# Optimization experiments

Measured on AMD Instinct MI355X. Metric: run time of the kernel, lower is better.

## Reference

```python
import jax, jax.numpy as jnp
import numpy as np

N_HEAD = 16

def setup_inputs() -> dict:
    key = jax.random.key(0)
    k1, k2, k3 = jax.random.split(key, 3)
    B, T, C = 2, 2048, 1024
    x_norm_for_qk = jax.random.normal(k1, (B, T, C), dtype=jnp.float32)
    xt_current_for_v = jax.random.normal(k2, (B, T, C), dtype=jnp.float32)
    W_attn = jax.random.normal(k3, (C, 2 * C), dtype=jnp.float32) * (1.0 / np.sqrt(C))
    b_attn = jnp.zeros((2 * C,), dtype=jnp.float32)
    return {"x_norm_for_qk": x_norm_for_qk, "xt_current_for_v": xt_current_for_v,
            "W_attn": W_attn, "b_attn": b_attn}

def reference(x_norm_for_qk, xt_current_for_v, W_attn, b_attn):
    B, T, C = x_norm_for_qk.shape
    H = N_HEAD
    D = C // H  # head dim
    qk = x_norm_for_qk @ W_attn + b_attn          # [B,T,2C]
    q, k = qk[..., :C], qk[..., C:]
    q = q.reshape(B, T, H, D).transpose(0, 2, 1, 3)   # [B,H,T,D]
    k = k.reshape(B, T, H, D).transpose(0, 2, 1, 3)
    v = xt_current_for_v.reshape(B, T, H, D).transpose(0, 2, 1, 3)
    scale = 1.0 / np.sqrt(D).astype(np.float32)
    scores = jnp.einsum('bhqd,bhkd->bhqk', q, k) * scale  # [B,H,T,T]
    causal = jnp.tril(jnp.ones((T, T), dtype=bool))
    scores = jnp.where(causal[None, None], scores, jnp.float32(-jnp.inf))
    weights = jax.nn.softmax(scores, axis=-1)  # dropout p=0.0 -> identity
    y = jnp.einsum('bhqk,bhkd->bhqd', weights, v)
    return y.transpose(0, 2, 1, 3).reshape(B, T, C)
```

## Files before the change

kernel.cpp:

```cpp
#include <hip/hip_runtime.h>
#include <hip/hip_bf16.h>
#include <math.h>

typedef __attribute__((ext_vector_type(8))) short s8v;
typedef __attribute__((ext_vector_type(4))) float f4v;
typedef __attribute__((ext_vector_type(16))) float f16v;
typedef __attribute__((ext_vector_type(2))) unsigned int u32x2;
typedef unsigned short ush;
typedef unsigned int u32;

#define QSCALE 0.180336880f
#define FIXED_M 10.0f

static __device__ __forceinline__ ush f2bf(float f) {
    u32 x = __builtin_bit_cast(u32, f);
    return (ush)((x + 0x7fffu + ((x >> 16) & 1u)) >> 16);
}
static __device__ __forceinline__ u32 bfpack(float lo, float hi) {
    u32 a = __builtin_bit_cast(u32, lo) + 0x8000u;
    u32 b = __builtin_bit_cast(u32, hi) + 0x8000u;
    return __builtin_amdgcn_perm(b, a, 0x07060302);
}
static __device__ __forceinline__ void gl_lds16(const void* g, void* l) {
    __builtin_amdgcn_global_load_lds(
        (const __attribute__((address_space(1))) u32*)g,
        (__attribute__((address_space(3))) u32*)l, 16, 0, 0);
}
#if __has_builtin(__builtin_amdgcn_exp2f)
#define EXP2F(x) __builtin_amdgcn_exp2f(x)
#else
#define EXP2F(x) exp2f(x)
#endif

static __device__ __forceinline__ void pl32swap(u32& a, u32& b) {
#if __has_builtin(__builtin_amdgcn_permlane32_swap)
    u32x2 r = __builtin_amdgcn_permlane32_swap(a, b, false, false);
    a = r[0]; b = r[1];
#else
    asm volatile("v_permlane32_swap_b32 %0, %1" : "+v"(a), "+v"(b));
#endif
}
static __device__ __forceinline__ s8v mkfrag(u32 a, u32 b, u32 c, u32 d) {
    union { u32 w[4]; s8v v; } u;
    u.w[0] = a; u.w[1] = b; u.w[2] = c; u.w[3] = d;
    return u.v;
}

static __device__ __forceinline__ void softpack(
    const f16v& s0, const f16v& s1, bool needmask, int kbase, int qg,
    float& lr, s8v& pf0, s8v& pf1, s8v& pf2, s8v& pf3)
{
    float ps = 0.f;
    u32 w0[4], w1[4], x0[4], x1[4];
    if (needmask) {
        #pragma unroll
        for (int g4 = 0; g4 < 4; ++g4) {
            const int kb0 = kbase + 8 * g4;
            float e0a = (kb0 + 0 > qg) ? 0.f : EXP2F(s0[g4 * 4 + 0] - FIXED_M);
            float e0b = (kb0 + 1 > qg) ? 0.f : EXP2F(s0[g4 * 4 + 1] - FIXED_M);
            float e0c = (kb0 + 2 > qg) ? 0.f : EXP2F(s0[g4 * 4 + 2] - FIXED_M);
            float e0d = (kb0 + 3 > qg) ? 0.f : EXP2F(s0[g4 * 4 + 3] - FIXED_M);
            float e1a = (kb0 + 32 > qg) ? 0.f : EXP2F(s1[g4 * 4 + 0] - FIXED_M);
            float e1b = (kb0 + 33 > qg) ? 0.f : EXP2F(s1[g4 * 4 + 1] - FIXED_M);
            float e1c = (kb0 + 34 > qg) ? 0.f : EXP2F(s1[g4 * 4 + 2] - FIXED_M);
            float e1d = (kb0 + 35 > qg) ? 0.f : EXP2F(s1[g4 * 4 + 3] - FIXED_M);
            ps += (e0a + e0b) + (e0c + e0d) + (e1a + e1b) + (e1c + e1d);
            w0[g4] = bfpack(e0a, e0b); w1[g4] = bfpack(e0c, e0d);
            x0[g4] = bfpack(e1a, e1b); x1[g4] = bfpack(e1c, e1d);
        }
    } else {
        #pragma unroll
        for (int g4 = 0; g4 < 4; ++g4) {
            float e0a = EXP2F(s0[g4 * 4 + 0] - FIXED_M);
            float e0b = EXP2F(s0[g4 * 4 + 1] - FIXED_M);
            float e0c = EXP2F(s0[g4 * 4 + 2] - FIXED_M);
            float e0d = EXP2F(s0[g4 * 4 + 3] - FIXED_M);
            float e1a = EXP2F(s1[g4 * 4 + 0] - FIXED_M);
            float e1b = EXP2F(s1[g4 * 4 + 1] - FIXED_M);
            float e1c = EXP2F(s1[g4 * 4 + 2] - FIXED_M);
            float e1d = EXP2F(s1[g4 * 4 + 3] - FIXED_M);
            ps += (e0a + e0b) + (e0c + e0d) + (e1a + e1b) + (e1c + e1d);
            w0[g4] = bfpack(e0a, e0b); w1[g4] = bfpack(e0c, e0d);
            x0[g4] = bfpack(e1a, e1b); x1[g4] = bfpack(e1c, e1d);
        }
    }
    ps += __shfl_xor(ps, 32);
    lr += ps;
    pl32swap(w0[0], w0[1]); pl32swap(w1[0], w1[1]);
    pl32swap(w0[2], w0[3]); pl32swap(w1[2], w1[3]);
    pl32swap(x0[0], x0[1]); pl32swap(x1[0], x1[1]);
    pl32swap(x0[2], x0[3]); pl32swap(x1[2], x1[3]);
    pf0 = mkfrag(w0[0], w1[0], w0[1], w1[1]);
    pf1 = mkfrag(w0[2], w1[2], w0[3], w1[3]);
    pf2 = mkfrag(x0[0], x1[0], x0[1], x1[1]);
    pf3 = mkfrag(x0[2], x1[2], x0[3], x1[3]);
}

__global__ __launch_bounds__(256) void prep_kernel(
    const float* __restrict__ X, const float* __restrict__ W,
    const float* __restrict__ XV,
    ush* __restrict__ Xb, ush* __restrict__ Wt, ush* __restrict__ Vtb)
{
    __shared__ float Ts[64][68];
    const int tid = threadIdx.x;
    const int bid = blockIdx.x;
    if (bid < 2048) {
        const size_t i = ((size_t)bid * 256 + tid) * 8;
        float4 v0 = *(const float4*)(X + i);
        float4 v1 = *(const float4*)(X + i + 4);
        uint4 o;
        o.x = bfpack(v0.x, v0.y); o.y = bfpack(v0.z, v0.w);
        o.z = bfpack(v1.x, v1.y); o.w = bfpack(v1.z, v1.w);
        *(uint4*)(Xb + i) = o;
    } else if (bid < 2560) {
        const int id = bid - 2048;
        const int n0 = (id & 31) * 64, k0 = (id >> 5) * 64;
        #pragma unroll
        for (int p = 0; p < 4; ++p) {
            const int idx = p * 256 + tid;
            const int kr = idx >> 4, nc4 = idx & 15;
            float4 v = *(const float4*)(W + (size_t)(k0 + kr) * 2048 + n0 + nc4 * 4);
            Ts[kr][nc4 * 4 + 0] = v.x; Ts[kr][nc4 * 4 + 1] = v.y;
            Ts[kr][nc4 * 4 + 2] = v.z; Ts[kr][nc4 * 4 + 3] = v.w;
        }
        __syncthreads();
        const int n = tid >> 2, kb = (tid & 3) * 16;
        #pragma unroll
        for (int p = 0; p < 4; ++p) {
            const int k = kb + p * 4;
            ushort4 o;
            o.x = f2bf(Ts[k + 0][n]); o.y = f2bf(Ts[k + 1][n]);
            o.z = f2bf(Ts[k + 2][n]); o.w = f2bf(Ts[k + 3][n]);
            *(ushort4*)(Wt + (size_t)(n0 + n) * 1024 + k0 + k) = o;
        }
    } else {
        const int id = bid - 2560;
        const int t0 = (id & 31) * 64;
        const int bh = id >> 5;
        const int b = bh >> 4, h = bh & 15;
        #pragma unroll
        for (int p = 0; p < 4; ++p) {
            const int idx = p * 256 + tid;
            const int tr = idx >> 4, dc4 = idx & 15;
            float4 v = *(const float4*)(XV + (size_t)(b * 2048 + t0 + tr) * 1024
                                        + h * 64 + dc4 * 4);
            Ts[tr][dc4 * 4 + 0] = v.x; Ts[tr][dc4 * 4 + 1] = v.y;
            Ts[tr][dc4 * 4 + 2] = v.z; Ts[tr][dc4 * 4 + 3] = v.w;
        }
        __syncthreads();
        const int d = tid >> 2, tb = (tid & 3) * 16;
        #pragma unroll
        for (int p = 0; p < 4; ++p) {
            const int tq = tb + p * 4;
            ushort4 o;
            o.x = f2bf(Ts[tq + 0][d]); o.y = f2bf(Ts[tq + 1][d]);
            o.z = f2bf(Ts[tq + 2][d]); o.w = f2bf(Ts[tq + 3][d]);
            *(ushort4*)(Vtb + (size_t)((b * 16 + h) * 64 + d) * 2048 + t0 + tq) = o;
        }
    }
}

__global__ __launch_bounds__(256) void gemm_kernel(
    const ush* __restrict__ Xb, const ush* __restrict__ Wt,
    const float* __restrict__ bias,
    ush* __restrict__ Qb, ush* __restrict__ Kb)
{
    __shared__ ush As[128 * 32];
    __shared__ ush Bs[128 * 32];

    const int tid = threadIdx.x;
    const int wid = tid >> 6, lane = tid & 63;
    const int quad = lane >> 4, l15 = lane & 15;
    const int wm = wid >> 1, wn = wid & 1;
    const int m0 = blockIdx.y * 128, n0 = blockIdx.x * 128;

    const int lrow = lane >> 2;
    const int lkk = (lane & 3) * 8;
    const size_t arow = (size_t)(m0 + wid * 32 + lrow);
    const size_t brow = (size_t)(n0 + wid * 32 + lrow);
    ush* AsW = &As[wid * 1024];
    ush* BsW = &Bs[wid * 1024];

    f4v acc[4][4];
    #pragma unroll
    for (int i = 0; i < 4; ++i)
        #pragma unroll
        for (int j = 0; j < 4; ++j) acc[i][j] = (f4v){0.f, 0.f, 0.f, 0.f};

    for (int k0 = 0; k0 < 1024; k0 += 32) {
        gl_lds16(Xb + arow * 1024 + k0 + lkk, AsW);
        gl_lds16(Xb + (arow + 16) * 1024 + k0 + lkk, AsW + 512);
        gl_lds16(Wt + brow * 1024 + k0 + lkk, BsW);
        gl_lds16(Wt + (brow + 16) * 1024 + k0 + lkk, BsW + 512);
        __syncthreads();

        s8v a[4], bf[4];
        #pragma unroll
        for (int i = 0; i < 4; ++i)
            a[i] = *(const s8v*)&As[(wm * 64 + i * 16 + l15) * 32 + quad * 8];
        #pragma unroll
        for (int j = 0; j < 4; ++j)
            bf[j] = *(const s8v*)&Bs[(wn * 64 + j * 16 + l15) * 32 + quad * 8];
        #pragma unroll
        for (int i = 0; i < 4; ++i)
            #pragma unroll
            for (int j = 0; j < 4; ++j)
                acc[i][j] = __builtin_amdgcn_mfma_f32_16x16x32_bf16(
                    a[i], bf[j], acc[i][j], 0, 0, 0);
        __syncthreads();
    }

    #pragma unroll
    for (int j = 0; j < 4; ++j) {
        const int n = n0 + wn * 64 + j * 16 + l15;
        const float bv = bias[n];
        const bool is_k = n >= 1024;
        const int nn = n & 1023;
        const int h = nn >> 6, d = nn & 63;
        ush* dst = is_k ? Kb : Qb;
        #pragma unroll
        for (int i = 0; i < 4; ++i) {
            const int mrow = m0 + wm * 64 + i * 16 + quad * 4;
            #pragma unroll
            for (int r = 0; r < 4; ++r) {
                const int m = mrow + r;
                const int b = m >> 11, t = m & 2047;
                float val = acc[i][j][r] + bv;
                if (!is_k) val *= QSCALE;
                dst[(size_t)((b * 16 + h) * 2048 + t) * 64 + d] = f2bf(val);
            }
        }
    }
}

__global__ __launch_bounds__(256, 2) void attn_kernel(
    const ush* __restrict__ Qb, const ush* __restrict__ Kb,
    const ush* __restrict__ Vt, float* __restrict__ Y)
{
    __shared__ ush SMEM[32768];
    ush* Kbuf = SMEM;
    ush* Vbuf = SMEM + 16384;

    const int tid = threadIdx.x;
    const int w = tid >> 6, lane = tid & 63;
    const int l31 = lane & 31, hi = lane >> 5;

    const int idx = blockIdx.x;
    const int half = idx >> 8, pair = idx & 255;
    const int qt = half ? (pair & 15) : 15 - (pair & 15);
    const int bh = (pair >> 4) + half * 16;
    const int b = bh >> 4, h = bh & 15;
    const int q0 = qt * 128;
    const int ktmax = 2 * qt + 1;

    const ush* Qg = Qb + (size_t)bh * 2048 * 64;
    const ush* Kg = Kb + (size_t)bh * 2048 * 64;
    const ush* Vg = Vt + (size_t)bh * 64 * 2048;

    ush* Pw = SMEM + w * 2304;
    {
        const int r8q = lane >> 3, c8 = lane & 7;
        #pragma unroll
        for (int p = 0; p < 4; ++p) {
            const int row = p * 8 + r8q;
            uint4 v = *(const uint4*)(Qg + (size_t)(q0 + w * 32 + row) * 64 + c8 * 8);
            *(uint4*)&Pw[row * 72 + c8 * 8] = v;
        }
    }
    s8v bq[4];
    #pragma unroll
    for (int s = 0; s < 4; ++s)
        bq[s] = *(const s8v*)&Pw[l31 * 72 + s * 16 + hi * 8];
    __syncthreads();

    const int r8 = lane >> 3;
    const int g8 = ((lane & 7) ^ r8) * 8;
    auto stage = [&](int kt) {
        const int buf = kt & 3;
        const int k0e = kt * 64;
        const ush* kg = Kg + (size_t)(k0e + w * 16 + r8) * 64 + g8;
        gl_lds16(kg, &Kbuf[buf * 4096 + (w * 16) * 64]);
        gl_lds16(kg + 8 * 64, &Kbuf[buf * 4096 + (w * 16 + 8) * 64]);
        const ush* vg = Vg + (size_t)(w * 16 + r8) * 2048 + k0e + g8;
        gl_lds16(vg, &Vbuf[buf * 4096 + (w * 16) * 64]);
        gl_lds16(vg + 8 * 2048, &Vbuf[buf * 4096 + (w * 16 + 8) * 64]);
    };

    f16v acco0 = {}, acco1 = {};
    float lr = 0.f;
    const int qg = q0 + w * 32 + l31;
    const int qwmax = q0 + w * 32 + 31;

    stage(0); stage(1);
    asm volatile("s_waitcnt vmcnt(4)" ::: "memory");
    __builtin_amdgcn_s_barrier();
    __builtin_amdgcn_sched_barrier(0);

    for (int kt = 0; kt <= ktmax; ++kt) {
        const int sl = (kt & 3) * 4096;
        const bool active = (kt * 64) <= qwmax;
        const bool pf = (kt + 2 <= ktmax);

        s8v ak0[4], ak1[4], av0[4], av1[4];
        if (active) {
            #pragma unroll
            for (int s = 0; s < 4; ++s) {
                const int ch = (s << 1) + hi;
                const int row0 = l31, row1 = 32 + l31;
                ak0[s] = *(const s8v*)&Kbuf[sl + row0 * 64 + ((ch ^ (row0 & 7)) << 3)];
                ak1[s] = *(const s8v*)&Kbuf[sl + row1 * 64 + ((ch ^ (row1 & 7)) << 3)];
                av0[s] = *(const s8v*)&Vbuf[sl + row0 * 64 + ((ch ^ (row0 & 7)) << 3)];
                av1[s] = *(const s8v*)&Vbuf[sl + row1 * 64 + ((ch ^ (row1 & 7)) << 3)];
            }
        }
        __builtin_amdgcn_sched_barrier(0);

        if (pf) stage(kt + 2);

        if (active) {
            f16v s0 = {}, s1 = {};
            #pragma unroll
            for (int s = 0; s < 4; ++s) {
                s0 = __builtin_amdgcn_mfma_f32_32x32x16_bf16(ak0[s], bq[s], s0, 0, 0, 0);
                s1 = __builtin_amdgcn_mfma_f32_32x32x16_bf16(ak1[s], bq[s], s1, 0, 0, 0);
            }

            s8v pf0, pf1, pf2, pf3;
            softpack(s0, s1, (kt * 64 + 63) > (q0 + w * 32),
                     kt * 64 + 4 * hi, qg, lr, pf0, pf1, pf2, pf3);

            acco0 = __builtin_amdgcn_mfma_f32_32x32x16_bf16(av0[0], pf0, acco0, 0, 0, 0);
            acco1 = __builtin_amdgcn_mfma_f32_32x32x16_bf16(av1[0], pf0, acco1, 0, 0, 0);
            acco0 = __builtin_amdgcn_mfma_f32_32x32x16_bf16(av0[1], pf1, acco0, 0, 0, 0);
            acco1 = __builtin_amdgcn_mfma_f32_32x32x16_bf16(av1[1], pf1, acco1, 0, 0, 0);
            acco0 = __builtin_amdgcn_mfma_f32_32x32x16_bf16(av0[2], pf2, acco0, 0, 0, 0);
            acco1 = __builtin_amdgcn_mfma_f32_32x32x16_bf16(av1[2], pf2, acco1, 0, 0, 0);
            acco0 = __builtin_amdgcn_mfma_f32_32x32x16_bf16(av0[3], pf3, acco0, 0, 0, 0);
            acco1 = __builtin_amdgcn_mfma_f32_32x32x16_bf16(av1[3], pf3, acco1, 0, 0, 0);
        }

        if (pf) asm volatile("s_waitcnt vmcnt(4)" ::: "memory");
        else    asm volatile("s_waitcnt vmcnt(0)" ::: "memory");
        __builtin_amdgcn_s_barrier();
        __builtin_amdgcn_sched_barrier(0);
    }

    float* LTw = (float*)SMEM + w * (32 * 68);
    const float inv = 1.0f / lr;
    #pragma unroll
    for (int r = 0; r < 16; ++r) {
        const int d = (r & 3) + 8 * (r >> 2) + 4 * hi;
        LTw[l31 * 68 + d] = acco0[r] * inv;
        LTw[l31 * 68 + 32 + d] = acco1[r] * inv;
    }
    const int qr4 = lane >> 4, chk = lane & 15;
    #pragma unroll
    for (int p = 0; p < 8; ++p) {
        const int qrow = p * 4 + qr4;
        f4v v = *(const f4v*)&LTw[qrow * 68 + chk * 4];
        *(float4*)(Y + (size_t)(b * 2048 + q0 + w * 32 + qrow) * 1024
                   + h * 64 + chk * 4) = (float4){v[0], v[1], v[2], v[3]};
    }
}

extern "C" void kernel_launch(void* const* d_in, const int* in_sizes, int n_in,
                              void* d_out, int out_size, void* d_ws,
                              size_t ws_size, hipStream_t stream)
{
    const float* x_qk = (const float*)d_in[0];
    const float* x_v  = (const float*)d_in[1];
    const float* W    = (const float*)d_in[2];
    const float* bias = (const float*)d_in[3];
    float* out = (float*)d_out;

    unsigned char* ws = (unsigned char*)d_ws;
    ush* Xb = (ush*)(ws);
    ush* Wt = (ush*)(ws + (8u << 20));
    ush* Qb = (ush*)(ws + (12u << 20));
    ush* Kb = (ush*)(ws + (20u << 20));
    ush* Vt = (ush*)(ws + (28u << 20));

    prep_kernel<<<3584, 256, 0, stream>>>(x_qk, W, x_v, Xb, Wt, Vt);
    gemm_kernel<<<dim3(16, 32), 256, 0, stream>>>(Xb, Wt, bias, Qb, Kb);
    attn_kernel<<<512, 256, 0, stream>>>(Qb, Kb, Vt, out);
}
```

Before: 148.7 us.

## Restructure attention into single-wave blocks loading K/V directly into registers

The attention kernel changes from 256-thread blocks with 128-query tiles and LDS-staged, 4-buffered K/V to 2048 one-wave blocks that each handle 32 queries. K and V fragments are now loaded straight from global memory into registers with a two-deep register double-buffer, which drops the LDS staging and block barriers. A new block-to-tile mapping interleaves long and short causal tiles to balance load. The trade-off is that K/V are no longer shared through LDS across waves, so global/L2 traffic per query rises, and the small blocks may hide latency less well.

```diff
diff --git a/kernel.cpp b/kernel.cpp
--- a/kernel.cpp
+++ b/kernel.cpp
@@ -44,56 +44,6 @@
     union { u32 w[4]; s8v v; } u;
     u.w[0] = a; u.w[1] = b; u.w[2] = c; u.w[3] = d;
     return u.v;
-}
-
-static __device__ __forceinline__ void softpack(
-    const f16v& s0, const f16v& s1, bool needmask, int kbase, int qg,
-    float& lr, s8v& pf0, s8v& pf1, s8v& pf2, s8v& pf3)
-{
-    float ps = 0.f;
-    u32 w0[4], w1[4], x0[4], x1[4];
-    if (needmask) {
-        #pragma unroll
-        for (int g4 = 0; g4 < 4; ++g4) {
-            const int kb0 = kbase + 8 * g4;
-            float e0a = (kb0 + 0 > qg) ? 0.f : EXP2F(s0[g4 * 4 + 0] - FIXED_M);
-            float e0b = (kb0 + 1 > qg) ? 0.f : EXP2F(s0[g4 * 4 + 1] - FIXED_M);
-            float e0c = (kb0 + 2 > qg) ? 0.f : EXP2F(s0[g4 * 4 + 2] - FIXED_M);
-            float e0d = (kb0 + 3 > qg) ? 0.f : EXP2F(s0[g4 * 4 + 3] - FIXED_M);
-            float e1a = (kb0 + 32 > qg) ? 0.f : EXP2F(s1[g4 * 4 + 0] - FIXED_M);
-            float e1b = (kb0 + 33 > qg) ? 0.f : EXP2F(s1[g4 * 4 + 1] - FIXED_M);
-            float e1c = (kb0 + 34 > qg) ? 0.f : EXP2F(s1[g4 * 4 + 2] - FIXED_M);
-            float e1d = (kb0 + 35 > qg) ? 0.f : EXP2F(s1[g4 * 4 + 3] - FIXED_M);
-            ps += (e0a + e0b) + (e0c + e0d) + (e1a + e1b) + (e1c + e1d);
-            w0[g4] = bfpack(e0a, e0b); w1[g4] = bfpack(e0c, e0d);
-            x0[g4] = bfpack(e1a, e1b); x1[g4] = bfpack(e1c, e1d);
-        }
-    } else {
-        #pragma unroll
-        for (int g4 = 0; g4 < 4; ++g4) {
-            float e0a = EXP2F(s0[g4 * 4 + 0] - FIXED_M);
-            float e0b = EXP2F(s0[g4 * 4 + 1] - FIXED_M);
-            float e0c = EXP2F(s0[g4 * 4 + 2] - FIXED_M);
-            float e0d = EXP2F(s0[g4 * 4 + 3] - FIXED_M);
-            float e1a = EXP2F(s1[g4 * 4 + 0] - FIXED_M);
-            float e1b = EXP2F(s1[g4 * 4 + 1] - FIXED_M);
-            float e1c = EXP2F(s1[g4 * 4 + 2] - FIXED_M);
-            float e1d = EXP2F(s1[g4 * 4 + 3] - FIXED_M);
-            ps += (e0a + e0b) + (e0c + e0d) + (e1a + e1b) + (e1c + e1d);
-            w0[g4] = bfpack(e0a, e0b); w1[g4] = bfpack(e0c, e0d);
-            x0[g4] = bfpack(e1a, e1b); x1[g4] = bfpack(e1c, e1d);
-        }
-    }
-    ps += __shfl_xor(ps, 32);
-    lr += ps;
-    pl32swap(w0[0], w0[1]); pl32swap(w1[0], w1[1]);
-    pl32swap(w0[2], w0[3]); pl32swap(w1[2], w1[3]);
-    pl32swap(x0[0], x0[1]); pl32swap(x1[0], x1[1]);
-    pl32swap(x0[2], x0[3]); pl32swap(x1[2], x1[3]);
-    pf0 = mkfrag(w0[0], w1[0], w0[1], w1[1]);
-    pf1 = mkfrag(w0[2], w1[2], w0[3], w1[3]);
-    pf2 = mkfrag(x0[0], x1[0], x0[1], x1[1]);
-    pf3 = mkfrag(x0[2], x1[2], x0[3], x1[3]);
 }
 
 __global__ __launch_bounds__(256) void prep_kernel(
@@ -233,132 +183,126 @@
     }
 }
 
-__global__ __launch_bounds__(256, 2) void attn_kernel(
+__global__ __launch_bounds__(64, 2) void attn_kernel(
     const ush* __restrict__ Qb, const ush* __restrict__ Kb,
     const ush* __restrict__ Vt, float* __restrict__ Y)
 {
-    __shared__ ush SMEM[32768];
-    ush* Kbuf = SMEM;
-    ush* Vbuf = SMEM + 16384;
-
-    const int tid = threadIdx.x;
-    const int w = tid >> 6, lane = tid & 63;
+    __shared__ float LT[32 * 68];
+
+    const int lane = threadIdx.x;
     const int l31 = lane & 31, hi = lane >> 5;
 
     const int idx = blockIdx.x;
-    const int half = idx >> 8, pair = idx & 255;
-    const int qt = half ? (pair & 15) : 15 - (pair & 15);
-    const int bh = (pair >> 4) + half * 16;
+    const int g = idx >> 8, c = idx & 255;
+    const int r = c & 7, bh = c >> 3;
+    const int qt = (g < 4) ? (63 - (4 * r + g)) : (4 * r + (g - 4));
     const int b = bh >> 4, h = bh & 15;
-    const int q0 = qt * 128;
-    const int ktmax = 2 * qt + 1;
+    const int q0 = qt * 32;
+    const int nt = qt + 1;
 
     const ush* Qg = Qb + (size_t)bh * 2048 * 64;
     const ush* Kg = Kb + (size_t)bh * 2048 * 64;
     const ush* Vg = Vt + (size_t)bh * 64 * 2048;
 
-    ush* Pw = SMEM + w * 2304;
+    s8v bq[4];
     {
-        const int r8q = lane >> 3, c8 = lane & 7;
-        #pragma unroll
-        for (int p = 0; p < 4; ++p) {
-            const int row = p * 8 + r8q;
-            uint4 v = *(const uint4*)(Qg + (size_t)(q0 + w * 32 + row) * 64 + c8 * 8);
-            *(uint4*)&Pw[row * 72 + c8 * 8] = v;
-        }
-    }
-    s8v bq[4];
-    #pragma unroll
-    for (int s = 0; s < 4; ++s)
-        bq[s] = *(const s8v*)&Pw[l31 * 72 + s * 16 + hi * 8];
-    __syncthreads();
-
-    const int r8 = lane >> 3;
-    const int g8 = ((lane & 7) ^ r8) * 8;
-    auto stage = [&](int kt) {
-        const int buf = kt & 3;
-        const int k0e = kt * 64;
-        const ush* kg = Kg + (size_t)(k0e + w * 16 + r8) * 64 + g8;
-        gl_lds16(kg, &Kbuf[buf * 4096 + (w * 16) * 64]);
-        gl_lds16(kg + 8 * 64, &Kbuf[buf * 4096 + (w * 16 + 8) * 64]);
-        const ush* vg = Vg + (size_t)(w * 16 + r8) * 2048 + k0e + g8;
-        gl_lds16(vg, &Vbuf[buf * 4096 + (w * 16) * 64]);
-        gl_lds16(vg + 8 * 2048, &Vbuf[buf * 4096 + (w * 16 + 8) * 64]);
+        const ush* qb = Qg + (size_t)(q0 + l31) * 64 + hi * 8;
+        bq[0] = *(const s8v*)(qb);
+        bq[1] = *(const s8v*)(qb + 16);
+        bq[2] = *(const s8v*)(qb + 32);
+        bq[3] = *(const s8v*)(qb + 48);
+    }
+
+    f16v acc0 = {}, acc1 = {};
+    float lr = 0.f;
+    const int qg = q0 + l31;
+
+    auto ldK = [&](int kt, s8v* ak) {
+        const ush* kb = Kg + (size_t)(kt * 32 + l31) * 64 + hi * 8;
+        ak[0] = *(const s8v*)(kb);
+        ak[1] = *(const s8v*)(kb + 16);
+        ak[2] = *(const s8v*)(kb + 32);
+        ak[3] = *(const s8v*)(kb + 48);
     };
-
-    f16v acco0 = {}, acco1 = {};
-    float lr = 0.f;
-    const int qg = q0 + w * 32 + l31;
-    const int qwmax = q0 + w * 32 + 31;
-
-    stage(0); stage(1);
-    asm volatile("s_waitcnt vmcnt(4)" ::: "memory");
-    __builtin_amdgcn_s_barrier();
-    __builtin_amdgcn_sched_barrier(0);
-
-    for (int kt = 0; kt <= ktmax; ++kt) {
-        const int sl = (kt & 3) * 4096;
-        const bool active = (kt * 64) <= qwmax;
-        const bool pf = (kt + 2 <= ktmax);
-
-        s8v ak0[4], ak1[4], av0[4], av1[4];
-        if (active) {
+    auto ldV = [&](int kt, s8v* av) {
+        const ush* vb0 = Vg + (size_t)l31 * 2048 + kt * 32 + hi * 8;
+        const ush* vb1 = vb0 + 32 * 2048;
+        av[0] = *(const s8v*)(vb0);
+        av[1] = *(const s8v*)(vb0 + 16);
+        av[2] = *(const s8v*)(vb1);
+        av[3] = *(const s8v*)(vb1 + 16);
+    };
+
+    auto comp = [&](int kt, const s8v* ak, const s8v* av) {
+        f16v s0 = {};
+        #pragma unroll
+        for (int s = 0; s < 4; ++s)
+            s0 = __builtin_amdgcn_mfma_f32_32x32x16_bf16(ak[s], bq[s], s0, 0, 0, 0);
+
+        float ps = 0.f;
+        u32 w0[4], w1[4];
+        if (kt == qt) {
+            const int kbase = kt * 32 + 4 * hi;
             #pragma unroll
-            for (int s = 0; s < 4; ++s) {
-                const int ch = (s << 1) + hi;
-                const int row0 = l31, row1 = 32 + l31;
-                ak0[s] = *(const s8v*)&Kbuf[sl + row0 * 64 + ((ch ^ (row0 & 7)) << 3)];
-                ak1[s] = *(const s8v*)&Kbuf[sl + row1 * 64 + ((ch ^ (row1 & 7)) << 3)];
-                av0[s] = *(const s8v*)&Vbuf[sl + row0 * 64 + ((ch ^ (row0 & 7)) << 3)];
-                av1[s] = *(const s8v*)&Vbuf[sl + row1 * 64 + ((ch ^ (row1 & 7)) << 3)];
+            for (int g4 = 0; g4 < 4; ++g4) {
+                const int kb0 = kbase + 8 * g4;
+                float e0a = (kb0 + 0 > qg) ? 0.f : EXP2F(s0[g4 * 4 + 0] - FIXED_M);
+                float e0b = (kb0 + 1 > qg) ? 0.f : EXP2F(s0[g4 * 4 + 1] - FIXED_M);
+                float e0c = (kb0 + 2 > qg) ? 0.f : EXP2F(s0[g4 * 4 + 2] - FIXED_M);
+                float e0d = (kb0 + 3 > qg) ? 0.f : EXP2F(s0[g4 * 4 + 3] - FIXED_M);
+                ps += (e0a + e0b) + (e0c + e0d);
+                w0[g4] = bfpack(e0a, e0b); w1[g4] = bfpack(e0c, e0d);
             }
-        }
-        __builtin_amdgcn_sched_barrier(0);
-
-        if (pf) stage(kt + 2);
-
-        if (active) {
-            f16v s0 = {}, s1 = {};
+        } else {
             #pragma unroll
-            for (int s = 0; s < 4; ++s) {
-                s0 = __builtin_amdgcn_mfma_f32_32x32x16_bf16(ak0[s], bq[s], s0, 0, 0, 0);
-                s1 = __builtin_amdgcn_mfma_f32_32x32x16_bf16(ak1[s], bq[s], s1, 0, 0, 0);
+            for (int g4 = 0; g4 < 4; ++g4) {
+                float e0a = EXP2F(s0[g4 * 4 + 0] - FIXED_M);
+                float e0b = EXP2F(s0[g4 * 4 + 1] - FIXED_M);
+                float e0c = EXP2F(s0[g4 * 4 + 2] - FIXED_M);
+                float e0d = EXP2F(s0[g4 * 4 + 3] - FIXED_M);
+                ps += (e0a + e0b) + (e0c + e0d);
+                w0[g4] = bfpack(e0a, e0b); w1[g4] = bfpack(e0c, e0d);
             }
-
-            s8v pf0, pf1, pf2, pf3;
-            softpack(s0, s1, (kt * 64 + 63) > (q0 + w * 32),
-                     kt * 64 + 4 * hi, qg, lr, pf0, pf1, pf2, pf3);
-
-            acco0 = __builtin_amdgcn_mfma_f32_32x32x16_bf16(av0[0], pf0, acco0, 0, 0, 0);
-            acco1 = __builtin_amdgcn_mfma_f32_32x32x16_bf16(av1[0], pf0, acco1, 0, 0, 0);
-            acco0 = __builtin_amdgcn_mfma_f32_32x32x16_bf16(av0[1], pf1, acco0, 0, 0, 0);
-            acco1 = __builtin_amdgcn_mfma_f32_32x32x16_bf16(av1[1], pf1, acco1, 0, 0, 0);
-            acco0 = __builtin_amdgcn_mfma_f32_32x32x16_bf16(av0[2], pf2, acco0, 0, 0, 0);
-            acco1 = __builtin_amdgcn_mfma_f32_32x32x16_bf16(av1[2], pf2, acco1, 0, 0, 0);
-            acco0 = __builtin_amdgcn_mfma_f32_32x32x16_bf16(av0[3], pf3, acco0, 0, 0, 0);
-            acco1 = __builtin_amdgcn_mfma_f32_32x32x16_bf16(av1[3], pf3, acco1, 0, 0, 0);
-        }
-
-        if (pf) asm volatile("s_waitcnt vmcnt(4)" ::: "memory");
-        else    asm volatile("s_waitcnt vmcnt(0)" ::: "memory");
-        __builtin_amdgcn_s_barrier();
-        __builtin_amdgcn_sched_barrier(0);
-    }
-
-    float* LTw = (float*)SMEM + w * (32 * 68);
+        }
+        ps += __shfl_xor(ps, 32);
+        lr += ps;
+
+        pl32swap(w0[0], w0[1]); pl32swap(w1[0], w1[1]);
+        pl32swap(w0[2], w0[3]); pl32swap(w1[2], w1[3]);
+        s8v pf0 = mkfrag(w0[0], w1[0], w0[1], w1[1]);
+        s8v pf1 = mkfrag(w0[2], w1[2], w0[3], w1[3]);
+
+        acc0 = __builtin_amdgcn_mfma_f32_32x32x16_bf16(av[0], pf0, acc0, 0, 0, 0);
+        acc1 = __builtin_amdgcn_mfma_f32_32x32x16_bf16(av[2], pf0, acc1, 0, 0, 0);
+        acc0 = __builtin_amdgcn_mfma_f32_32x32x16_bf16(av[1], pf1, acc0, 0, 0, 0);
+        acc1 = __builtin_amdgcn_mfma_f32_32x32x16_bf16(av[3], pf1, acc1, 0, 0, 0);
+    };
+
+    s8v akA[4], avA[4], akB[4], avB[4];
+    ldK(0, akA); ldV(0, avA);
+    for (int kt = 0; kt < nt; kt += 2) {
+        const bool hasB = (kt + 1 < nt);
+        if (hasB) { ldK(kt + 1, akB); ldV(kt + 1, avB); }
+        comp(kt, akA, avA);
+        if (hasB) {
+            if (kt + 2 < nt) { ldK(kt + 2, akA); ldV(kt + 2, avA); }
+            comp(kt + 1, akB, avB);
+        }
+    }
+
     const float inv = 1.0f / lr;
     #pragma unroll
-    for (int r = 0; r < 16; ++r) {
-        const int d = (r & 3) + 8 * (r >> 2) + 4 * hi;
-        LTw[l31 * 68 + d] = acco0[r] * inv;
-        LTw[l31 * 68 + 32 + d] = acco1[r] * inv;
+    for (int r2 = 0; r2 < 16; ++r2) {
+        const int d = (r2 & 3) + 8 * (r2 >> 2) + 4 * hi;
+        LT[l31 * 68 + d] = acc0[r2] * inv;
+        LT[l31 * 68 + 32 + d] = acc1[r2] * inv;
     }
     const int qr4 = lane >> 4, chk = lane & 15;
     #pragma unroll
     for (int p = 0; p < 8; ++p) {
         const int qrow = p * 4 + qr4;
-        f4v v = *(const f4v*)&LTw[qrow * 68 + chk * 4];
-        *(float4*)(Y + (size_t)(b * 2048 + q0 + w * 32 + qrow) * 1024
+        f4v v = *(const f4v*)&LT[qrow * 68 + chk * 4];
+        *(float4*)(Y + (size_t)(b * 2048 + q0 + qrow) * 1024
                    + h * 64 + chk * 4) = (float4){v[0], v[1], v[2], v[3]};
     }
 }
@@ -382,5 +326,5 @@
 
     prep_kernel<<<3584, 256, 0, stream>>>(x_qk, W, x_v, Xb, Wt, Vt);
     gemm_kernel<<<dim3(16, 32), 256, 0, stream>>>(Xb, Wt, bias, Qb, Kb);
-    attn_kernel<<<512, 256, 0, stream>>>(Qb, Kb, Vt, out);
-}
+    attn_kernel<<<2048, 64, 0, stream>>>(Qb, Kb, Vt, out);
+}
```

Measured after the change: 180.9 us. 21.7% more time.

## Multi-buffer GEMM LDS tiles and prefetch two k-steps ahead

Applied to the files above, without the earlier changes.

Replaces the single-buffered load/sync/compute loop of the QK projection GEMM with a 4-slot LDS ring that issues global-to-LDS loads two iterations ahead and waits with explicit vmcnt counters and one barrier per step. The goal is to overlap global memory latency with MFMA work. It raises LDS use to 64KB per block and adds launch bounds of 2 blocks per CU, which may limit occupancy or register allocation. Correctness depends on the hand-tuned waitcnt values matching the number of outstanding loads.

```diff
diff --git a/kernel.cpp b/kernel.cpp
--- a/kernel.cpp
+++ b/kernel.cpp
@@ -160,13 +160,13 @@
     }
 }
 
-__global__ __launch_bounds__(256) void gemm_kernel(
+__global__ __launch_bounds__(256, 2) void gemm_kernel(
     const ush* __restrict__ Xb, const ush* __restrict__ Wt,
     const float* __restrict__ bias,
     ush* __restrict__ Qb, ush* __restrict__ Kb)
 {
-    __shared__ ush As[128 * 32];
-    __shared__ ush Bs[128 * 32];
+    __shared__ ush As[4][128 * 32];
+    __shared__ ush Bs[4][128 * 32];
 
     const int tid = threadIdx.x;
     const int wid = tid >> 6, lane = tid & 63;
@@ -178,8 +178,14 @@
     const int lkk = (lane & 3) * 8;
     const size_t arow = (size_t)(m0 + wid * 32 + lrow);
     const size_t brow = (size_t)(n0 + wid * 32 + lrow);
-    ush* AsW = &As[wid * 1024];
-    ush* BsW = &Bs[wid * 1024];
+
+    auto stage = [&](int k) {
+        const int k0 = k * 32, sl = k & 3;
+        gl_lds16(Xb + arow * 1024 + k0 + lkk, &As[sl][wid * 1024]);
+        gl_lds16(Xb + (arow + 16) * 1024 + k0 + lkk, &As[sl][wid * 1024 + 512]);
+        gl_lds16(Wt + brow * 1024 + k0 + lkk, &Bs[sl][wid * 1024]);
+        gl_lds16(Wt + (brow + 16) * 1024 + k0 + lkk, &Bs[sl][wid * 1024 + 512]);
+    };
 
     f4v acc[4][4];
     #pragma unroll
@@ -187,27 +193,37 @@
         #pragma unroll
         for (int j = 0; j < 4; ++j) acc[i][j] = (f4v){0.f, 0.f, 0.f, 0.f};
 
-    for (int k0 = 0; k0 < 1024; k0 += 32) {
-        gl_lds16(Xb + arow * 1024 + k0 + lkk, AsW);
-        gl_lds16(Xb + (arow + 16) * 1024 + k0 + lkk, AsW + 512);
-        gl_lds16(Wt + brow * 1024 + k0 + lkk, BsW);
-        gl_lds16(Wt + (brow + 16) * 1024 + k0 + lkk, BsW + 512);
-        __syncthreads();
+    stage(0); stage(1);
+    asm volatile("s_waitcnt vmcnt(4)" ::: "memory");
+    __builtin_amdgcn_s_barrier();
+    __builtin_amdgcn_sched_barrier(0);
+
+    for (int k = 0; k < 32; ++k) {
+        const int sl = k & 3;
+        const bool pf = (k + 2 < 32);
 
         s8v a[4], bf[4];
         #pragma unroll
         for (int i = 0; i < 4; ++i)
-            a[i] = *(const s8v*)&As[(wm * 64 + i * 16 + l15) * 32 + quad * 8];
+            a[i] = *(const s8v*)&As[sl][(wm * 64 + i * 16 + l15) * 32 + quad * 8];
         #pragma unroll
         for (int j = 0; j < 4; ++j)
-            bf[j] = *(const s8v*)&Bs[(wn * 64 + j * 16 + l15) * 32 + quad * 8];
+            bf[j] = *(const s8v*)&Bs[sl][(wn * 64 + j * 16 + l15) * 32 + quad * 8];
+        __builtin_amdgcn_sched_barrier(0);
+
+        if (pf) stage(k + 2);
+
         #pragma unroll
         for (int i = 0; i < 4; ++i)
             #pragma unroll
             for (int j = 0; j < 4; ++j)
                 acc[i][j] = __builtin_amdgcn_mfma_f32_16x16x32_bf16(
                     a[i], bf[j], acc[i][j], 0, 0, 0);
-        __syncthreads();
+
+        if (pf) asm volatile("s_waitcnt vmcnt(4)" ::: "memory");
+        else    asm volatile("s_waitcnt vmcnt(0)" ::: "memory");
+        __builtin_amdgcn_s_barrier();
+        __builtin_amdgcn_sched_barrier(0);
     }
 
     #pragma unroll
```

Result: faster. 145.5 us (-2.1%).
